# Kernel optimization log

Measured on AMD Instinct MI355X. Metric: run time of the kernel, lower is better.

Reference implementation:

```python
import jax, jax.numpy as jnp
import numpy as np

B, I, C, L, KS = 16, 64, 128, 16384, 5
CA_K = 5
K_CR = 76      # crucial channels: floor(0.6*128)=76, already even
EPS = 1e-5


def conv1d(x, w, pad):
    # x: [N, Cin, L], w: [Cout, Cin, K]
    return jax.lax.conv_general_dilated(
        x, w, window_strides=(1,), padding=[(pad, pad)],
        dimension_numbers=('NCH', 'OIH', 'NCH'))


def bn(x, g, b, m, v):
    # eval-mode BatchNorm1d over channel dim of [N, C, L]
    inv = g / jnp.sqrt(v + EPS)
    return x * inv[None, :, None] + (b - m * inv)[None, :, None]


def setup_inputs() -> dict:
    key = jax.random.key(0)
    ks = jax.random.split(key, 10)
    return {
        'x': jax.random.normal(ks[0], (B, I, L), jnp.float32),
        'conv_w': jax.random.normal(ks[1], (C, I, KS), jnp.float32) / np.sqrt(I * KS).astype(np.float32),
        'conv_b': jax.random.normal(ks[2], (C,), jnp.float32) * 0.01,
        'bn_g': jnp.ones((C,), jnp.float32) + jax.random.normal(ks[3], (C,), jnp.float32) * 0.05,
        'bn_b': jax.random.normal(ks[4], (C,), jnp.float32) * 0.05,
        'bn_m': jax.random.normal(ks[5], (C,), jnp.float32) * 0.05,
        'bn_v': jnp.ones((C,), jnp.float32) + jax.random.uniform(ks[6], (C,), jnp.float32) * 0.1,
        'alpha': jnp.float32(0.5),
        'beta': jnp.float32(0.5),
        'ca_w': jax.random.normal(ks[7], (1, 1, CA_K), jnp.float32) / np.sqrt(CA_K).astype(np.float32),
        'ca_b': jnp.zeros((1,), jnp.float32),
        'sa_w': jax.random.normal(ks[8], (1, 2, 7), jnp.float32) / np.sqrt(14.0).astype(np.float32),
        'sabn_g': jnp.ones((1,), jnp.float32) + jax.random.normal(ks[9], (1,), jnp.float32) * 0.05,
        'sabn_b': jnp.zeros((1,), jnp.float32),
        'sabn_m': jnp.zeros((1,), jnp.float32),
        'sabn_v': jnp.ones((1,), jnp.float32),
    }


def reference(x, conv_w, conv_b, bn_g, bn_b, bn_m, bn_v, alpha, beta,
              ca_w, ca_b, sa_w, sabn_g, sabn_b, sabn_m, sabn_v):
    # ---- conv_layer: Conv1d + BN + ReLU ----
    f = conv1d(x, conv_w, KS // 2) + conv_b[None, :, None]      # [B,C,L]
    f = jax.nn.relu(bn(f, bn_g, bn_b, bn_m, bn_v))

    # ---- ChannelAttention ----
    F_avg = jnp.mean(f, axis=2, keepdims=True)                  # [B,C,1]
    F_max = jnp.max(f, axis=2, keepdims=True)                   # [B,C,1]
    F_add = alpha * F_avg + 0.5 * (F_avg + F_max) + beta * F_max
    z = conv1d(F_add.transpose(0, 2, 1), ca_w, CA_K // 2) + ca_b[None, :, None]  # [B,1,C]
    channel_map = jax.nn.sigmoid(z.transpose(0, 2, 1))          # [B,C,1]

    crf = f * channel_map                                       # channel refined features

    # ---- SpatialAttention: topk channel split + scatter masks ----
    cm = channel_map[:, :, 0]                                   # [B,C]
    _, idx = jax.lax.top_k(cm, K_CR)                            # [B,K_CR]
    cru = jnp.zeros_like(cm).at[jnp.arange(B)[:, None], idx].set(1.0)[:, :, None]  # [B,C,1]
    sub = 1.0 - cru

    cf = cru * crf                                              # crucial features [B,C,L]
    sf = sub * crf                                              # subcrucial features

    c_max = jnp.max(cf, axis=1, keepdims=True)                  # [B,1,L]
    c_avg = jnp.mean(cf, axis=1, keepdims=True) * (C / K_CR)
    s_max = jnp.max(sf, axis=1, keepdims=True)
    s_avg = jnp.mean(sf, axis=1, keepdims=True) * (C / (C - K_CR))

    def gate(mx, av):
        y = conv1d(jnp.concatenate([mx, av], axis=1), sa_w, 3)  # [B,1,L]
        return jax.nn.sigmoid(jax.nn.relu(bn(y, sabn_g, sabn_b, sabn_m, sabn_v)))

    A1 = gate(c_max, c_avg)
    A2 = gate(s_max, s_avg)
    return cf * A1 + sf * A2                                    # [B,C,L]
```

## Files before the change

### kernel.cpp

```cpp
#include <hip/hip_runtime.h>
#include <hip/hip_bf16.h>
#include <math.h>

#define BB 16
#define IC 64
#define CH 128
#define LL 16384
#define KS 5
#define CAK 5
#define KCR 76
#define EPSV 1e-5f
#define NLT2 256
#define EPSR 8e-3f

typedef _Float16 f16x8 __attribute__((ext_vector_type(8)));
typedef float f32x16 __attribute__((ext_vector_type(16)));

#define OFF_WPACK 0
#define OFF_W2F   20480
#define OFF_BIAS2 (OFF_W2F + 40960)
#define OFF_PSUM  (OFF_BIAS2 + CH)
#define OFF_PMAX  (OFF_PSUM + BB*CH*NLT2)
#define OFF_FADD  (OFF_PMAX + BB*CH*NLT2)
#define OFF_CM    (OFF_FADD + BB*CH)
#define OFF_MASK  (OFF_CM + BB*CH)
#define OFF_F16   (OFF_MASK + BB*CH)

__device__ __forceinline__ unsigned short f2h(float f) {
    _Float16 h = (_Float16)f;
    return __builtin_bit_cast(unsigned short, h);
}
__device__ __forceinline__ float h2f(unsigned short u) {
    _Float16 h = __builtin_bit_cast(_Float16, u);
    return (float)h;
}

template<int CTRL>
__device__ __forceinline__ float dppf(float v) {
    return __builtin_bit_cast(float,
        __builtin_amdgcn_update_dpp(0, __builtin_bit_cast(int, v), CTRL, 0xF, 0xF, true));
}
__device__ __forceinline__ float dpp_sum32(float s) {
    s += dppf<0x111>(s);
    s += dppf<0x112>(s);
    s += dppf<0x114>(s);
    s += dppf<0x118>(s);
    s += dppf<0x142>(s);
    return s;
}
__device__ __forceinline__ float dpp_max32(float m) {
    m = fmaxf(m, dppf<0x111>(m));
    m = fmaxf(m, dppf<0x112>(m));
    m = fmaxf(m, dppf<0x114>(m));
    m = fmaxf(m, dppf<0x118>(m));
    m = fmaxf(m, dppf<0x142>(m));
    return m;
}

__global__ void prep_kernel(const float* __restrict__ conv_w, const float* __restrict__ conv_b,
                            const float* __restrict__ bn_g, const float* __restrict__ bn_b,
                            const float* __restrict__ bn_m, const float* __restrict__ bn_v,
                            unsigned short* __restrict__ wpack, float* __restrict__ w2f,
                            float* __restrict__ bias2)
{
    int e = blockIdx.x * 256 + threadIdx.x;
    if (e < 4 * 20 * 64 * 8) {
        int j    = e & 7;
        int ln   = (e >> 3) & 63;
        int rest = e >> 9;
        int s    = rest % 20;
        int mt   = (rest / 20) & 1;
        int ch2  = rest / 40;
        int c  = ch2 * 64 + mt * 32 + (ln & 31);
        int kk = s >> 2;
        int i  = (s & 3) * 16 + (ln >> 5) * 8 + j;
        float inv = bn_g[c] * rsqrtf(bn_v[c] + EPSV);
        wpack[e] = f2h(conv_w[(c * IC + i) * KS + kk] * inv);
    }
    if (e < CH * KS * IC) {
        int i  = e & 63;
        int kk = (e >> 6) % KS;
        int c  = e / (KS * IC);
        float inv = bn_g[c] * rsqrtf(bn_v[c] + EPSV);
        w2f[e] = conv_w[(c * IC + i) * KS + kk] * inv;
    }
    if (e < CH) {
        float inv = bn_g[e] * rsqrtf(bn_v[e] + EPSV);
        bias2[e] = (conv_b[e] - bn_m[e]) * inv + bn_b[e];
    }
}

__global__ __launch_bounds__(256, 4)
void conv_mfma_kernel(const float* __restrict__ x,
                      const unsigned short* __restrict__ wpack,
                      const float* __restrict__ bias2,
                      unsigned short* __restrict__ f16,
                      float* __restrict__ psum, float* __restrict__ pmax)
{
    __shared__ unsigned short xs[136 * 64];
    const int b   = blockIdx.x;
    const int lt  = blockIdx.y;
    const int l0  = lt * 128;
    const int tid = threadIdx.x;
    const int ln  = tid & 63;
    const int wv  = __builtin_amdgcn_readfirstlane(tid >> 6);

    const float* xb = x + (size_t)b * (IC * LL);
    const int ibase = wv * 16;
    #pragma unroll
    for (int g = 0; g < 3; ++g) {
        int row = g * 64 + ln;
        int l   = l0 - 4 + row;
        if (row < 136) {
            bool vl = (l >= 0) && (l < LL);
            float v[16];
            #pragma unroll
            for (int q = 0; q < 16; ++q)
                v[q] = vl ? xb[(size_t)(ibase + q) * LL + l] : 0.0f;
            unsigned short h[16];
            #pragma unroll
            for (int q = 0; q < 16; ++q) h[q] = f2h(v[q]);
            int rs = row & 7;
            #pragma unroll
            for (int q2 = 0; q2 < 2; ++q2) {
                int i0    = ibase + q2 * 8;
                int chunk = (i0 >> 3) ^ rs;
                uint4 w4;
                w4.x = (unsigned)h[q2*8+0] | ((unsigned)h[q2*8+1] << 16);
                w4.y = (unsigned)h[q2*8+2] | ((unsigned)h[q2*8+3] << 16);
                w4.z = (unsigned)h[q2*8+4] | ((unsigned)h[q2*8+5] << 16);
                w4.w = (unsigned)h[q2*8+6] | ((unsigned)h[q2*8+7] << 16);
                *(uint4*)&xs[row * 64 + chunk * 8] = w4;
            }
        }
    }
    __syncthreads();

    const int ch2  = wv >> 1;
    const int lh   = wv & 1;
    const int ln31 = ln & 31;
    const int hi   = ln >> 5;
    const int rowbase = lh * 64 + ln31 + 2;

    const unsigned short* wp  = wpack + (size_t)ln * 8;
    const unsigned short* pA0 = wp + (size_t)((ch2 * 2 + 0) * 20) * 512;
    const unsigned short* pA1 = wp + (size_t)((ch2 * 2 + 1) * 20) * 512;

    f32x16 acc[2][2];
    #pragma unroll
    for (int mt = 0; mt < 2; ++mt)
        #pragma unroll
        for (int nt = 0; nt < 2; ++nt)
            #pragma unroll
            for (int r = 0; r < 16; ++r) acc[mt][nt][r] = 0.0f;

    auto loadA = [&](f16x8* Av, int s) {
        Av[0] = *(const f16x8*)(pA0 + (size_t)s * 512);
        Av[1] = *(const f16x8*)(pA1 + (size_t)s * 512);
    };
    auto loadB = [&](f16x8* Bv, int s) {
        int kk = s >> 2, iq = s & 3;
        int r0 = rowbase + kk;
        int r1 = r0 + 32;
        int c0 = ((iq << 1) + hi) ^ (r0 & 7);
        int c1 = ((iq << 1) + hi) ^ (r1 & 7);
        Bv[0] = *(const f16x8*)&xs[r0 * 64 + c0 * 8];
        Bv[1] = *(const f16x8*)&xs[r1 * 64 + c1 * 8];
    };
    auto compute = [&](const f16x8* Av, const f16x8* Bv) {
        acc[0][0] = __builtin_amdgcn_mfma_f32_32x32x16_f16(Av[0], Bv[0], acc[0][0], 0, 0, 0);
        acc[1][0] = __builtin_amdgcn_mfma_f32_32x32x16_f16(Av[1], Bv[0], acc[1][0], 0, 0, 0);
        acc[0][1] = __builtin_amdgcn_mfma_f32_32x32x16_f16(Av[0], Bv[1], acc[0][1], 0, 0, 0);
        acc[1][1] = __builtin_amdgcn_mfma_f32_32x32x16_f16(Av[1], Bv[1], acc[1][1], 0, 0, 0);
    };

    f16x8 Ar[2][2], Br[2][2];
    loadA(Ar[0], 0); loadB(Br[0], 0);
    #pragma unroll
    for (int s = 0; s < 20; ++s) {
        if (s + 1 < 20) { loadA(Ar[(s + 1) & 1], s + 1); loadB(Br[(s + 1) & 1], s + 1); }
        compute(Ar[s & 1], Br[s & 1]);
    }

    const int lgbase = l0 + lh * 64 + ln31;
    #pragma unroll
    for (int mt = 0; mt < 2; ++mt) {
        #pragma unroll
        for (int nt = 0; nt < 2; ++nt) {
            #pragma unroll
            for (int r = 0; r < 16; ++r) {
                int c = ch2 * 64 + mt * 32 + (r & 3) + 8 * (r >> 2) + 4 * hi;
                float fv = fmaxf(acc[mt][nt][r] + bias2[c], 0.0f);
                f16[((size_t)(b * CH + c)) * LL + lgbase + nt * 32] = f2h(fv);
                acc[mt][nt][r] = fv;
            }
        }
    }
    #pragma unroll
    for (int mt = 0; mt < 2; ++mt) {
        #pragma unroll
        for (int r = 0; r < 16; ++r) {
            float s = dpp_sum32(acc[mt][0][r] + acc[mt][1][r]);
            float m = dpp_max32(fmaxf(acc[mt][0][r], acc[mt][1][r]));
            if (ln31 == 31) {
                int c   = ch2 * 64 + mt * 32 + (r & 3) + 8 * (r >> 2) + 4 * hi;
                int lt2 = lt * 2 + lh;
                psum[(b * CH + c) * NLT2 + lt2] = s;
                pmax[(b * CH + c) * NLT2 + lt2] = m;
            }
        }
    }
}

__global__ __launch_bounds__(64)
void fixmax_kernel(const float* __restrict__ x, const float* __restrict__ w2f,
                   const float* __restrict__ bias2,
                   const float* __restrict__ psum, const float* __restrict__ pmax,
                   const float* __restrict__ alpha, const float* __restrict__ beta,
                   float* __restrict__ fadd)
{
    const int c  = blockIdx.x;
    const int b  = blockIdx.y;
    const int ln = threadIdx.x;
    const float* ps = psum + (size_t)(b * CH + c) * NLT2;
    const float* pm = pmax + (size_t)(b * CH + c) * NLT2;

    float pmg[4], s4 = 0.0f, m4 = 0.0f;
    #pragma unroll
    for (int g = 0; g < 4; ++g) {
        pmg[g] = pm[g * 64 + ln];
        s4 += ps[g * 64 + ln];
        m4 = fmaxf(m4, pmg[g]);
    }
    float stot = s4, M = m4;
    #pragma unroll
    for (int off = 1; off <= 32; off <<= 1) {
        stot += __shfl_xor(stot, off, 64);
        M = fmaxf(M, __shfl_xor(M, off, 64));
    }

    const float* xb  = x + (size_t)b * (IC * LL);
    const float* w2c = w2f + (size_t)c * (KS * IC);
    const float bsc  = bias2[c];
    float Fmax = 0.0f;
    int cnt = 0;
    #pragma unroll
    for (int g = 0; g < 4 && cnt < 8; ++g) {
        unsigned long long bal = __ballot(pmg[g] >= M - EPSR);
        while (bal && cnt < 8) {
            int sl = __ffsll((long long)bal) - 1;
            bal &= bal - 1;
            ++cnt;
            int slot = g * 64 + sl;
            int l    = (slot >> 1) * 128 + (slot & 1) * 64 + ln;
            float fe = bsc;
            #pragma unroll
            for (int kk = 0; kk < KS; ++kk) {
                int lidx = l + kk - 2;
                bool v = (lidx >= 0) && (lidx < LL);
                const float* xr = xb + lidx;
                const float* wr = w2c + kk * IC;
                for (int i = 0; i < IC; ++i) {
                    float xv = v ? xr[(size_t)i * LL] : 0.0f;
                    fe = fmaf(xv, wr[i], fe);
                }
            }
            fe = fmaxf(fe, 0.0f);
            #pragma unroll
            for (int off = 1; off <= 32; off <<= 1)
                fe = fmaxf(fe, __shfl_xor(fe, off, 64));
            Fmax = fmaxf(Fmax, fe);
        }
    }

    if (ln == 0) {
        float favg = stot * (1.0f / LL);
        fadd[b * CH + c] = (alpha[0] + 0.5f) * favg + (beta[0] + 0.5f) * Fmax;
    }
}

__global__ void chan2_kernel(const float* __restrict__ fadd,
                             const float* __restrict__ ca_w, const float* __restrict__ ca_b,
                             float* __restrict__ cm, float* __restrict__ maskv)
{
    int b = blockIdx.x;
    int c = threadIdx.x;
    __shared__ float fa[CH];
    __shared__ float cms[CH];
    fa[c] = fadd[b * CH + c];
    __syncthreads();

    float z = ca_b[0];
    #pragma unroll
    for (int k = 0; k < CAK; ++k) {
        int cc = c + k - 2;
        float v = (cc >= 0 && cc < CH) ? fa[cc] : 0.0f;
        z = fmaf(ca_w[k], v, z);
    }
    float cmv = 1.0f / (1.0f + expf(-z));
    cms[c] = cmv;
    __syncthreads();

    int rank = 0;
    for (int cc = 0; cc < CH; ++cc) {
        float o = cms[cc];
        rank += (o > cmv || (o == cmv && cc < c)) ? 1 : 0;
    }
    cm[b * CH + c] = cmv;
    maskv[b * CH + c] = (rank < KCR) ? 1.0f : 0.0f;
}

__global__ __launch_bounds__(256)
void sgf_kernel(const unsigned short* __restrict__ f16, float* __restrict__ out,
                const float* __restrict__ cm, const float* __restrict__ maskv,
                const float* __restrict__ sa_w,
                const float* __restrict__ sabn_g, const float* __restrict__ sabn_b,
                const float* __restrict__ sabn_m, const float* __restrict__ sabn_v)
{
    __shared__ float cms[CH], mks[CH];
    __shared__ float st[4][520];
    const int g   = blockIdx.x;
    const int b   = blockIdx.y;
    const int l0  = g * 512;
    const int tid = threadIdx.x;
    if (tid < CH) { cms[tid] = cm[b * CH + tid]; mks[tid] = maskv[b * CH + tid]; }
    __syncthreads();

    {
        const unsigned short* fb = f16 + (size_t)b * CH * LL + l0 + 2 * tid;
        float cmx0 = 0.f, csm0 = 0.f, smx0 = 0.f, ssm0 = 0.f;
        float cmx1 = 0.f, csm1 = 0.f, smx1 = 0.f, ssm1 = 0.f;
        #pragma unroll 4
        for (int c = 0; c < CH; ++c) {
            unsigned pr = *(const unsigned*)(fb + (size_t)c * LL);
            float cmc = cms[c], mk = mks[c];
            float v0 = h2f((unsigned short)(pr & 0xFFFFu)) * cmc;
            float v1 = h2f((unsigned short)(pr >> 16)) * cmc;
            float vs0 = v0 * mk, vu0 = v0 - vs0;
            float vs1 = v1 * mk, vu1 = v1 - vs1;
            cmx0 = fmaxf(cmx0, vs0); smx0 = fmaxf(smx0, vu0); csm0 += vs0; ssm0 += vu0;
            cmx1 = fmaxf(cmx1, vs1); smx1 = fmaxf(smx1, vu1); csm1 += vs1; ssm1 += vu1;
        }
        int s0 = 3 + 2 * tid;
        st[0][s0] = cmx0;                  st[0][s0 + 1] = cmx1;
        st[1][s0] = csm0 * (1.0f / KCR);   st[1][s0 + 1] = csm1 * (1.0f / KCR);
        st[2][s0] = smx0;                  st[2][s0 + 1] = smx1;
        st[3][s0] = ssm0 * (1.0f / (CH - KCR));
        st[3][s0 + 1] = ssm1 * (1.0f / (CH - KCR));
    }
    if (tid < 6) {
        int slot = (tid < 3) ? tid : 515 + (tid - 3);
        int l = l0 - 3 + slot;
        float cmx = 0.f, csm = 0.f, smx = 0.f, ssm = 0.f;
        if (l >= 0 && l < LL) {
            const unsigned short* fb = f16 + (size_t)b * CH * LL + l;
            for (int c = 0; c < CH; ++c) {
                float v  = h2f(fb[(size_t)c * LL]) * cms[c];
                float mk = mks[c];
                float vs = v * mk, vu = v - vs;
                cmx = fmaxf(cmx, vs); smx = fmaxf(smx, vu);
                csm += vs; ssm += vu;
            }
        }
        st[0][slot] = cmx;
        st[1][slot] = csm * (1.0f / KCR);
        st[2][slot] = smx;
        st[3][slot] = ssm * (1.0f / (CH - KCR));
    }
    __syncthreads();

    float inv = sabn_g[0] * rsqrtf(sabn_v[0] + EPSV);
    float bb2 = sabn_b[0] - sabn_m[0] * inv;
    float y1a = 0.f, y2a = 0.f, y1b = 0.f, y2b = 0.f;
    #pragma unroll
    for (int k = 0; k < 7; ++k) {
        float wm = sa_w[k], wa = sa_w[7 + k];
        int s0 = 2 * tid + k;
        y1a = fmaf(wm, st[0][s0],     fmaf(wa, st[1][s0],     y1a));
        y2a = fmaf(wm, st[2][s0],     fmaf(wa, st[3][s0],     y2a));
        y1b = fmaf(wm, st[0][s0 + 1], fmaf(wa, st[1][s0 + 1], y1b));
        y2b = fmaf(wm, st[2][s0 + 1], fmaf(wa, st[3][s0 + 1], y2b));
    }
    float A1a = 1.0f / (1.0f + expf(-fmaxf(y1a * inv + bb2, 0.f)));
    float A2a = 1.0f / (1.0f + expf(-fmaxf(y2a * inv + bb2, 0.f)));
    float A1b = 1.0f / (1.0f + expf(-fmaxf(y1b * inv + bb2, 0.f)));
    float A2b = 1.0f / (1.0f + expf(-fmaxf(y2b * inv + bb2, 0.f)));

    const unsigned short* fb = f16 + (size_t)b * CH * LL + l0 + 2 * tid;
    float* ob = out + (size_t)b * CH * LL + l0 + 2 * tid;
    #pragma unroll 4
    for (int c = 0; c < CH; ++c) {
        unsigned pr = *(const unsigned*)(fb + (size_t)c * LL);
        float cmc = cms[c];
        float v0 = h2f((unsigned short)(pr & 0xFFFFu)) * cmc;
        float v1 = h2f((unsigned short)(pr >> 16)) * cmc;
        bool sel = (mks[c] > 0.5f);
        float2 w;
        w.x = v0 * (sel ? A1a : A2a);
        w.y = v1 * (sel ? A1b : A2b);
        *(float2*)(ob + (size_t)c * LL) = w;
    }
}

extern "C" void kernel_launch(void* const* d_in, const int* in_sizes, int n_in,
                              void* d_out, int out_size, void* d_ws, size_t ws_size,
                              hipStream_t stream)
{
    const float* x      = (const float*)d_in[0];
    const float* conv_w = (const float*)d_in[1];
    const float* conv_b = (const float*)d_in[2];
    const float* bn_g   = (const float*)d_in[3];
    const float* bn_b   = (const float*)d_in[4];
    const float* bn_m   = (const float*)d_in[5];
    const float* bn_v   = (const float*)d_in[6];
    const float* alpha  = (const float*)d_in[7];
    const float* beta   = (const float*)d_in[8];
    const float* ca_w   = (const float*)d_in[9];
    const float* ca_b   = (const float*)d_in[10];
    const float* sa_w   = (const float*)d_in[11];
    const float* sabn_g = (const float*)d_in[12];
    const float* sabn_b = (const float*)d_in[13];
    const float* sabn_m = (const float*)d_in[14];
    const float* sabn_v = (const float*)d_in[15];

    float* out = (float*)d_out;
    float* ws  = (float*)d_ws;

    unsigned short* wpack = (unsigned short*)(ws + OFF_WPACK);
    float* w2f   = ws + OFF_W2F;
    float* bias2 = ws + OFF_BIAS2;
    float* psum  = ws + OFF_PSUM;
    float* pmax  = ws + OFF_PMAX;
    float* faddp = ws + OFF_FADD;
    float* cmv_  = ws + OFF_CM;
    float* mskv  = ws + OFF_MASK;
    unsigned short* f16p = (unsigned short*)(ws + OFF_F16);

    prep_kernel<<<160, 256, 0, stream>>>(conv_w, conv_b, bn_g, bn_b, bn_m, bn_v,
                                         wpack, w2f, bias2);

    conv_mfma_kernel<<<dim3(BB, 128), 256, 0, stream>>>(x, wpack, bias2, f16p, psum, pmax);

    fixmax_kernel<<<dim3(CH, BB), 64, 0, stream>>>(x, w2f, bias2, psum, pmax,
                                                   alpha, beta, faddp);

    chan2_kernel<<<BB, CH, 0, stream>>>(faddp, ca_w, ca_b, cmv_, mskv);

    sgf_kernel<<<dim3(32, BB), 256, 0, stream>>>(f16p, out, cmv_, mskv, sa_w,
                                                 sabn_g, sabn_b, sabn_m, sabn_v);
}
```

Baseline: 193.2 us.

## Parallelize fixmax candidate recomputation across four waves with shared candidate list

```diff
diff --git a/kernel.cpp b/kernel.cpp
--- a/kernel.cpp
+++ b/kernel.cpp
@@ -11,7 +11,7 @@
 #define KCR 76
 #define EPSV 1e-5f
 #define NLT2 256
-#define EPSR 8e-3f
+#define EPSR 5e-3f
 
 typedef _Float16 f16x8 __attribute__((ext_vector_type(8)));
 typedef float f32x16 __attribute__((ext_vector_type(16)));
@@ -212,68 +212,73 @@
     }
 }
 
-__global__ __launch_bounds__(64)
+__global__ __launch_bounds__(256)
 void fixmax_kernel(const float* __restrict__ x, const float* __restrict__ w2f,
                    const float* __restrict__ bias2,
                    const float* __restrict__ psum, const float* __restrict__ pmax,
                    const float* __restrict__ alpha, const float* __restrict__ beta,
                    float* __restrict__ fadd)
 {
-    const int c  = blockIdx.x;
-    const int b  = blockIdx.y;
-    const int ln = threadIdx.x;
+    __shared__ float wm[4], wsum[4], wfm[4];
+    __shared__ int candList[NLT2];
+    __shared__ int ncand;
+    const int c   = blockIdx.x;
+    const int b   = blockIdx.y;
+    const int tid = threadIdx.x;
+    const int ln  = tid & 63;
+    const int wv  = tid >> 6;
+
     const float* ps = psum + (size_t)(b * CH + c) * NLT2;
     const float* pm = pmax + (size_t)(b * CH + c) * NLT2;
-
-    float pmg[4], s4 = 0.0f, m4 = 0.0f;
-    #pragma unroll
-    for (int g = 0; g < 4; ++g) {
-        pmg[g] = pm[g * 64 + ln];
-        s4 += ps[g * 64 + ln];
-        m4 = fmaxf(m4, pmg[g]);
-    }
-    float stot = s4, M = m4;
+    float pmv = pm[tid];
+    float psv = ps[tid];
+
+    float m = pmv, s = psv;
     #pragma unroll
     for (int off = 1; off <= 32; off <<= 1) {
-        stot += __shfl_xor(stot, off, 64);
-        M = fmaxf(M, __shfl_xor(M, off, 64));
-    }
+        s += __shfl_xor(s, off, 64);
+        m = fmaxf(m, __shfl_xor(m, off, 64));
+    }
+    if (tid == 0) ncand = 0;
+    if (ln == 0) { wm[wv] = m; wsum[wv] = s; }
+    __syncthreads();
+    float M    = fmaxf(fmaxf(wm[0], wm[1]), fmaxf(wm[2], wm[3]));
+    float stot = (wsum[0] + wsum[1]) + (wsum[2] + wsum[3]);
+
+    if (pmv >= M - EPSR) { int k = atomicAdd(&ncand, 1); candList[k] = tid; }
+    __syncthreads();
+    const int nc = ncand;
 
     const float* xb  = x + (size_t)b * (IC * LL);
     const float* w2c = w2f + (size_t)c * (KS * IC);
     const float bsc  = bias2[c];
-    float Fmax = 0.0f;
-    int cnt = 0;
-    #pragma unroll
-    for (int g = 0; g < 4 && cnt < 8; ++g) {
-        unsigned long long bal = __ballot(pmg[g] >= M - EPSR);
-        while (bal && cnt < 8) {
-            int sl = __ffsll((long long)bal) - 1;
-            bal &= bal - 1;
-            ++cnt;
-            int slot = g * 64 + sl;
-            int l    = (slot >> 1) * 128 + (slot & 1) * 64 + ln;
-            float fe = bsc;
-            #pragma unroll
-            for (int kk = 0; kk < KS; ++kk) {
-                int lidx = l + kk - 2;
-                bool v = (lidx >= 0) && (lidx < LL);
-                const float* xr = xb + lidx;
-                const float* wr = w2c + kk * IC;
-                for (int i = 0; i < IC; ++i) {
-                    float xv = v ? xr[(size_t)i * LL] : 0.0f;
-                    fe = fmaf(xv, wr[i], fe);
-                }
+    float Fm = 0.0f;
+    for (int k = wv; k < nc; k += 4) {
+        int slot = candList[k];
+        int l    = (slot >> 1) * 128 + (slot & 1) * 64 + ln;
+        float fe = bsc;
+        #pragma unroll
+        for (int kk = 0; kk < KS; ++kk) {
+            int lidx = l + kk - 2;
+            bool v = (lidx >= 0) && (lidx < LL);
+            const float* xr = xb + lidx;
+            const float* wr = w2c + kk * IC;
+            #pragma unroll 16
+            for (int i = 0; i < IC; ++i) {
+                float xv = v ? xr[(size_t)i * LL] : 0.0f;
+                fe = fmaf(xv, wr[i], fe);
             }
-            fe = fmaxf(fe, 0.0f);
-            #pragma unroll
-            for (int off = 1; off <= 32; off <<= 1)
-                fe = fmaxf(fe, __shfl_xor(fe, off, 64));
-            Fmax = fmaxf(Fmax, fe);
-        }
-    }
-
-    if (ln == 0) {
+        }
+        fe = fmaxf(fe, 0.0f);
+        #pragma unroll
+        for (int off = 1; off <= 32; off <<= 1)
+            fe = fmaxf(fe, __shfl_xor(fe, off, 64));
+        Fm = fmaxf(Fm, fe);
+    }
+    if (ln == 0) wfm[wv] = Fm;
+    __syncthreads();
+    if (tid == 0) {
+        float Fmax = fmaxf(fmaxf(wfm[0], wfm[1]), fmaxf(wfm[2], wfm[3]));
         float favg = stot * (1.0f / LL);
         fadd[b * CH + c] = (alpha[0] + 0.5f) * favg + (beta[0] + 0.5f) * Fmax;
     }
@@ -441,8 +446,8 @@
 
     conv_mfma_kernel<<<dim3(BB, 128), 256, 0, stream>>>(x, wpack, bias2, f16p, psum, pmax);
 
-    fixmax_kernel<<<dim3(CH, BB), 64, 0, stream>>>(x, w2f, bias2, psum, pmax,
-                                                   alpha, beta, faddp);
+    fixmax_kernel<<<dim3(CH, BB), 256, 0, stream>>>(x, w2f, bias2, psum, pmax,
+                                                    alpha, beta, faddp);
 
     chan2_kernel<<<BB, CH, 0, stream>>>(faddp, ca_w, ca_b, cmv_, mskv);
 
```

New measurement: 180.6 us. 6.5% less time.
